# Optimization experiments

Measured on AMD Instinct MI355X. Metric: run time of the kernel, lower is better.

## Reference

```python
import jax, jax.numpy as jnp
import numpy as np

B, L, D_MODEL, N_HEADS = 2, 2048, 1024, 16
D_HEAD = D_MODEL // N_HEADS
EPS = 1e-5


def setup_inputs() -> dict:
    key = jax.random.key(0)
    ks = jax.random.split(key, 10)
    x = jax.random.normal(ks[0], (B, L, D_MODEL), dtype=jnp.float32)
    # causal boolean mask [B, L, L]
    attn_mask = jnp.broadcast_to(jnp.tril(jnp.ones((L, L), dtype=bool)), (B, L, L))
    ts = jax.random.randint(ks[1], (B, L), 0, 10000)
    rope_lambda = jax.random.uniform(ks[2], (B, L, 1), dtype=jnp.float32)
    q_gate = jax.random.uniform(ks[3], (B, L, N_HEADS), dtype=jnp.float32)
    k_gate = jax.random.uniform(ks[4], (B, L, N_HEADS), dtype=jnp.float32)
    v_gate = jax.random.uniform(ks[5], (B, L, N_HEADS), dtype=jnp.float32)
    type_pair_bias = jax.random.normal(ks[6], (B, 1, L, L), dtype=jnp.float32)
    # parameters (torch Linear convention: y = x @ W.T + b)
    proj_w = jax.random.normal(ks[7], (4 * D_MODEL, D_MODEL), dtype=jnp.float32) * 0.02
    proj_b = jnp.zeros((4 * D_MODEL,), dtype=jnp.float32)
    out_w = jax.random.normal(ks[8], (D_MODEL, D_MODEL), dtype=jnp.float32) * 0.02
    out_b = jnp.zeros((D_MODEL,), dtype=jnp.float32)
    head_scale = jnp.ones((N_HEADS,), dtype=jnp.float32) * (D_HEAD ** -0.5)
    ln_gamma = jnp.ones((D_MODEL,), dtype=jnp.float32)
    ln_beta = jnp.zeros((D_MODEL,), dtype=jnp.float32)
    return {"x": x, "attn_mask": attn_mask, "ts": ts, "rope_lambda": rope_lambda,
            "q_gate": q_gate, "k_gate": k_gate, "v_gate": v_gate,
            "type_pair_bias": type_pair_bias, "proj_w": proj_w, "proj_b": proj_b,
            "out_w": out_w, "out_b": out_b, "head_scale": head_scale,
            "ln_gamma": ln_gamma, "ln_beta": ln_beta}


def _split_heads(t):
    b, l, _ = t.shape
    return t.reshape(b, l, N_HEADS, D_HEAD).transpose(0, 2, 1, 3)  # [B,H,L,Dh]


def _apply_rope(q, k, rope_lambda):
    # behavior-module RoPE: positions from cumsum of rope_lambda
    pos = jnp.cumsum(rope_lambda[..., 0], axis=1)  # [B, L]
    inv_freq = 1.0 / (10000.0 ** (jnp.arange(0, D_HEAD, 2, dtype=jnp.float32) / D_HEAD))
    freqs = pos[:, None, :, None] * inv_freq[None, None, None, :]  # [B,1,L,Dh/2]
    cos, sin = jnp.cos(freqs), jnp.sin(freqs)

    def rot(t):
        te, to = t[..., 0::2], t[..., 1::2]
        return jnp.concatenate([te * cos - to * sin, te * sin + to * cos], axis=-1)

    return rot(q), rot(k)


def reference(x, attn_mask, ts, rope_lambda, q_gate, k_gate, v_gate,
              type_pair_bias, proj_w, proj_b, out_w, out_b, head_scale,
              ln_gamma, ln_beta):
    b, l, d = x.shape
    h = jax.nn.silu(x @ proj_w.T + proj_b)  # [B,L,4D]
    u, v, q, k = jnp.split(h, 4, axis=-1)
    u, v, q, k = _split_heads(u), _split_heads(v), _split_heads(q), _split_heads(k)
    q, k = _apply_rope(q, k, rope_lambda)
    # multiplicative per-head gates: [B,L,H] -> [B,H,L,1]
    q = q * q_gate.transpose(0, 2, 1)[..., None]
    k = k * k_gate.transpose(0, 2, 1)[..., None]
    v = v * v_gate.transpose(0, 2, 1)[..., None]
    logits = jnp.einsum('bhid,bhjd->bhij', q, k)
    logits = logits * head_scale[None, :, None, None]
    # original does two adds: + type_pair_bias and + 3.0 * type_pair_bias
    logits = logits + type_pair_bias
    logits = logits + 3.0 * type_pair_bias
    logits = jax.nn.silu(logits)  # non-softmax SiLU attention
    logits = jnp.where(attn_mask[:, None, :, :], logits, 0.0)
    y = jnp.einsum('bhij,bhjd->bhid', logits, v)  # [B,H,L,Dh]
    y = y.transpose(0, 2, 1, 3).reshape(b, l, d)
    y = y * u.transpose(0, 2, 1, 3).reshape(b, l, d)  # gated output
    y = y @ out_w.T + out_b
    r = x + y  # dropout is identity in eval mode
    mu = jnp.mean(r, axis=-1, keepdims=True)
    var = jnp.mean((r - mu) ** 2, axis=-1, keepdims=True)
    return (r - mu) / jnp.sqrt(var + EPS) * ln_gamma + ln_beta
```

## Files before the change

kernel.cpp:

```cpp
#include <hip/hip_runtime.h>
#include <cstdint>
#include <cstddef>

typedef unsigned short u16;
typedef __attribute__((ext_vector_type(8))) short short8v;
typedef __attribute__((ext_vector_type(4))) float f32x4;

#define B_   2
#define L_   2048
#define D_   1024
#define NH_  16
#define DH_  64
#define M_   (B_*L_)
#define N4_  (4*D_)

__device__ __forceinline__ float bf2f(u16 u) {
  union { float f; unsigned int i; } v; v.i = ((unsigned int)u) << 16; return v.f;
}
__device__ __forceinline__ u16 f2bf(float f) {
  union { float f; unsigned int i; } v; v.f = f;
  unsigned int x = v.i;
  return (u16)((x + 0x7fffu + ((x >> 16) & 1u)) >> 16);
}
__device__ __forceinline__ unsigned int pk_bf16(float a, float b) {
#if __has_builtin(__builtin_amdgcn_cvt_pk_bf16_f32)
  auto r = __builtin_amdgcn_cvt_pk_bf16_f32(a, b);
  union { decltype(r) v; unsigned int u; } c; c.v = r; return c.u;
#else
  unsigned int r;
  asm("v_cvt_pk_bf16_f32 %0, %1, %2" : "=v"(r) : "v"(a), "v"(b));
  return r;
#endif
}
__device__ __forceinline__ float siluf(float x) {
  return x * __builtin_amdgcn_rcpf(1.0f + __expf(-x));
}

__device__ __forceinline__ void gl2lds16(const u16* g, u16* l) {
  __builtin_amdgcn_global_load_lds(
      (const __attribute__((address_space(1))) unsigned int*)(const void*)g,
      (__attribute__((address_space(3))) unsigned int*)(void*)l,
      16, 0, 0);
}

__global__ __launch_bounds__(256) void k_conv_cum(const float* __restrict__ x,
                                                  const float* __restrict__ pw,
                                                  const float* __restrict__ ow,
                                                  const float* __restrict__ lam,
                                                  u16* __restrict__ xb,
                                                  u16* __restrict__ pwb,
                                                  u16* __restrict__ owb,
                                                  float* __restrict__ pos) {
  const int NX = M_ * D_ / 4, NP = N4_ * D_ / 4;
  int bid = blockIdx.x;
  int tid = threadIdx.x;
  if (bid < 9216) {
    int i = bid * 256 + tid;
    const float* src; u16* dst; int j;
    if (i < NX)            { src = x;  dst = xb;  j = i; }
    else if (i < NX + NP)  { src = pw; dst = pwb; j = i - NX; }
    else                   { src = ow; dst = owb; j = i - NX - NP; }
    float4 v = ((const float4*)src)[j];
    ushort4 o; o.x = f2bf(v.x); o.y = f2bf(v.y); o.z = f2bf(v.z); o.w = f2bf(v.w);
    ((ushort4*)dst)[j] = o;
  } else {
    int b = bid - 9216;
    const float* in = lam + (size_t)b * L_;
    float* out = pos + (size_t)b * L_;
    float loc[8], s = 0.0f;
#pragma unroll
    for (int i = 0; i < 8; ++i) { loc[i] = in[tid * 8 + i]; s += loc[i]; }
    __shared__ float sb[256];
    sb[tid] = s;
    __syncthreads();
    for (int off = 1; off < 256; off <<= 1) {
      float t = (tid >= off) ? sb[tid - off] : 0.0f;
      __syncthreads();
      sb[tid] += t;
      __syncthreads();
    }
    float run = sb[tid] - s;
#pragma unroll
    for (int i = 0; i < 8; ++i) { run += loc[i]; out[tid * 8 + i] = run; }
  }
}

__global__ __launch_bounds__(256, 4) void k_gemm1(const u16* __restrict__ A,
                                                  const u16* __restrict__ Bw,
                                                  const float* __restrict__ bias,
                                                  u16* __restrict__ hu, u16* __restrict__ hv,
                                                  u16* __restrict__ hq, u16* __restrict__ hk) {
  const int K = D_;
  int bn = blockIdx.x, bm = blockIdx.y, tid = threadIdx.x;
  int w = tid >> 6, lane = tid & 63, quad = lane >> 4, r16 = lane & 15;
  __shared__ __align__(16) u16 As[8192], Bs[8192];
  const u16* gA = A  + (size_t)(bm * 128) * K;
  const u16* gB = Bw + (size_t)(bn * 128) * K;
  int srow = tid >> 2, sc = tid & 3;
#pragma unroll
  for (int s = 0; s < 2; ++s) {
    int row = s * 64 + srow;
    int q = (sc - (row >> 1)) & 3;
    gl2lds16(gA + (size_t)row * K + q * 8, As + s * 2048 + w * 512);
    gl2lds16(gB + (size_t)row * K + q * 8, Bs + s * 2048 + w * 512);
  }
  f32x4 acc[4][4] = {};
  int wm = w & 1, wn = w >> 1;
  const int rowb = wm * 64, colb = wn * 64;
  for (int n = 0; n < 32; ++n) {
    __syncthreads();
    if (n + 1 < 32) {
      int kt = (n + 1) * 32, pb = (n + 1) & 1;
#pragma unroll
      for (int s = 0; s < 2; ++s) {
        int row = s * 64 + srow;
        int q = (sc - (row >> 1)) & 3;
        gl2lds16(gA + (size_t)row * K + kt + q * 8, As + pb * 4096 + s * 2048 + w * 512);
        gl2lds16(gB + (size_t)row * K + kt + q * 8, Bs + pb * 4096 + s * 2048 + w * 512);
      }
    }
    const u16* Ab = As + (n & 1) * 4096;
    const u16* Bb = Bs + (n & 1) * 4096;
    short8v af[4], bf[4];
#pragma unroll
    for (int mi = 0; mi < 4; ++mi) {
      int row = rowb + mi * 16 + r16;
      af[mi] = *(const short8v*)(Ab + (row * 4 + ((quad + (row >> 1)) & 3)) * 8);
    }
#pragma unroll
    for (int ni = 0; ni < 4; ++ni) {
      int row = colb + ni * 16 + r16;
      bf[ni] = *(const short8v*)(Bb + (row * 4 + ((quad + (row >> 1)) & 3)) * 8);
    }
#pragma unroll
    for (int mi = 0; mi < 4; ++mi)
#pragma unroll
      for (int ni = 0; ni < 4; ++ni)
        acc[mi][ni] = __builtin_amdgcn_mfma_f32_16x16x32_bf16(af[mi], bf[ni], acc[mi][ni], 0, 0, 0);
  }
  int nb = (bn * 128) >> 10;
  u16* dst = (nb == 0) ? hu : (nb == 1) ? hv : (nb == 2) ? hq : hk;
  int cbase = (bn * 128) & 1023;
  int row0 = bm * 128 + rowb;
#pragma unroll
  for (int ni = 0; ni < 4; ++ni) {
    int gcol = bn * 128 + colb + ni * 16 + r16;
    int lcol = cbase + colb + ni * 16 + r16;
    float bb = bias[gcol];
#pragma unroll
    for (int mi = 0; mi < 4; ++mi)
#pragma unroll
      for (int r = 0; r < 4; ++r) {
        int row = row0 + mi * 16 + quad * 4 + r;
        dst[(size_t)row * D_ + lcol] = f2bf(siluf(acc[mi][ni][r] + bb));
      }
  }
}

__global__ __launch_bounds__(256) void k_rope_vt(const u16* __restrict__ hq, const u16* __restrict__ hk,
                                                 const u16* __restrict__ hv,
                                                 const float* __restrict__ pos,
                                                 const float* __restrict__ qg, const float* __restrict__ kg,
                                                 const float* __restrict__ vg,
                                                 const float* __restrict__ hsc,
                                                 u16* __restrict__ Qb, u16* __restrict__ Kb,
                                                 u16* __restrict__ Vtb) {
  int bid = blockIdx.x;
  int tid = threadIdx.x;
  if (bid < 2048) {
    int idx = bid * 256 + tid;
    int j4 = idx & 7;
    int l  = (idx >> 3) & 2047;
    int bh = idx >> 14;
    int b = bh >> 4, hh = bh & 15;
    int row = b * L_ + l;
    float p = pos[row];
    float qs = qg[(size_t)row * NH_ + hh] * hsc[hh];
    float kgv = kg[(size_t)row * NH_ + hh];
    const u16* hqr = hq + (size_t)row * D_ + hh * DH_ + j4 * 8;
    const u16* hkr = hk + (size_t)row * D_ + hh * DH_ + j4 * 8;
    short8v qv = *(const short8v*)hqr;
    short8v kv = *(const short8v*)hkr;
    size_t ob = ((size_t)bh * L_ + l) * DH_ + j4 * 4;
    u16 qeo[4], qoo[4], keo[4], koo[4];
#pragma unroll
    for (int t = 0; t < 4; ++t) {
      int j = j4 * 4 + t;
      float inv = __expf(-(float)j * 0.28782313662425574f);
      float a = p * inv;
      float c, s;
      __sincosf(a, &s, &c);
      float qe = bf2f((u16)qv[2 * t]), qo = bf2f((u16)qv[2 * t + 1]);
      float ke = bf2f((u16)kv[2 * t]), ko = bf2f((u16)kv[2 * t + 1]);
      qeo[t] = f2bf((qe * c - qo * s) * qs);
      qoo[t] = f2bf((qe * s + qo * c) * qs);
      keo[t] = f2bf((ke * c - ko * s) * kgv);
      koo[t] = f2bf((ke * s + ko * c) * kgv);
    }
    *(ushort4*)(Qb + ob)      = make_ushort4(qeo[0], qeo[1], qeo[2], qeo[3]);
    *(ushort4*)(Qb + ob + 32) = make_ushort4(qoo[0], qoo[1], qoo[2], qoo[3]);
    *(ushort4*)(Kb + ob)      = make_ushort4(keo[0], keo[1], keo[2], keo[3]);
    *(ushort4*)(Kb + ob + 32) = make_ushort4(koo[0], koo[1], koo[2], koo[3]);
  } else {
    int b2 = bid - 2048;
    int lt = b2 & 31;
    int bh = b2 >> 5;
    int b = bh >> 4, hh = bh & 15;
    __shared__ u16 t[64][68];
    {
      int r = tid >> 2, cg = tid & 3;
      int row = b * L_ + lt * 64 + r;
      float gv = vg[(size_t)row * NH_ + hh];
      const u16* src = hv + (size_t)row * D_ + hh * DH_ + cg * 16;
      short8v v0 = ((const short8v*)src)[0];
      short8v v1 = ((const short8v*)src)[1];
#pragma unroll
      for (int e = 0; e < 8; ++e) {
        t[r][cg * 16 + e]     = f2bf(bf2f((u16)v0[e]) * gv);
        t[r][cg * 16 + 8 + e] = f2bf(bf2f((u16)v1[e]) * gv);
      }
    }
    __syncthreads();
    {
      int d = tid >> 2, lg = tid & 3;
      short8v o0, o1;
#pragma unroll
      for (int e = 0; e < 8; ++e) o0[e] = (short)t[lg * 16 + e][d];
#pragma unroll
      for (int e = 0; e < 8; ++e) o1[e] = (short)t[lg * 16 + 8 + e][d];
      u16* dst = Vtb + ((size_t)bh * DH_ + d) * L_ + lt * 64 + lg * 16;
      ((short8v*)dst)[0] = o0;
      ((short8v*)dst)[1] = o1;
    }
  }
}

__global__ __launch_bounds__(256, 4) void k_attn(const u16* __restrict__ Qb, const u16* __restrict__ Kb,
                                                 const u16* __restrict__ Vtb, const float* __restrict__ tpb,
                                                 const u16* __restrict__ hu, u16* __restrict__ A2) {
  int id = blockIdx.x;
  int group = id >> 5, bh = id & 31;
  int i64 = (group & 1) ? (group >> 1) : (31 - (group >> 1));
  int jmax = i64 >> 1;
  int b = bh >> 4, hh = bh & 15;
  int tid = threadIdx.x, w = tid >> 6, lane = tid & 63, quad = lane >> 4, r16 = lane & 15;
  __shared__ __align__(16) u16 Ks[8192];
  __shared__ __align__(16) u16 Vs[8192];
  const size_t bhbase = (size_t)bh * L_ * DH_;
  int irow = i64 * 64 + w * 16;
  int gimax_w = irow + 15;
  const u16* qt = Qb + bhbase + (size_t)irow * DH_;
  short8v bq[2];
#pragma unroll
  for (int ks = 0; ks < 2; ++ks)
    bq[ks] = *(const short8v*)(qt + (size_t)r16 * DH_ + ks * 32 + quad * 8);
#pragma unroll
  for (int s = 0; s < 4; ++s) {
    int row = (s & 1) * 64 + (tid >> 2);
    int q = ((tid & 3) - (row >> 1)) & 3;
    gl2lds16(Kb + bhbase + (size_t)row * DH_ + (s >> 1) * 32 + q * 8, Ks + s * 2048 + w * 512);
  }
  const float* bpr = tpb + ((size_t)b * L_ + irow + r16) * L_ + quad * 4;
  float4 bv[8];
#pragma unroll
  for (int tj = 0; tj < 8; ++tj)
    if (tj * 16 <= gimax_w) bv[tj] = *(const float4*)(bpr + tj * 16);
  f32x4 accy[4] = {};
  for (int jt = 0; jt <= jmax; ++jt) {
    __syncthreads();
#pragma unroll
    for (int s = 0; s < 4; ++s) {
      int row = tid >> 2;
      int q = ((tid & 3) - (row >> 1)) & 3;
      gl2lds16(Vtb + bhbase + (size_t)row * L_ + jt * 128 + s * 32 + q * 8, Vs + s * 2048 + w * 512);
    }
    unsigned int paw[4][4];
#pragma unroll
    for (int ks2 = 0; ks2 < 4; ++ks2) {
      if (jt * 128 + ks2 * 32 > gimax_w) continue;
      unsigned int W[2][2];
#pragma unroll
      for (int t = 0; t < 2; ++t) {
        int tj = 2 * ks2 + t;
        int jlo = jt * 128 + tj * 16;
        unsigned int p01 = 0, p23 = 0;
        if (jlo <= gimax_w) {
          int row = tj * 16 + r16;
          int sw = (quad + (row >> 1)) & 3;
          short8v ak0 = *(const short8v*)(Ks + (row * 4 + sw) * 8);
          short8v ak1 = *(const short8v*)(Ks + 4096 + (row * 4 + sw) * 8);
          f32x4 acc = {};
          acc = __builtin_amdgcn_mfma_f32_16x16x32_bf16(ak0, bq[0], acc, 0, 0, 0);
          acc = __builtin_amdgcn_mfma_f32_16x16x32_bf16(ak1, bq[1], acc, 0, 0, 0);
          int gi = irow + r16;
          int j0 = jlo + quad * 4;
          float4 bvv = bv[tj];
          float v0 = (j0     <= gi) ? siluf(fmaf(4.0f, bvv.x, acc[0])) : 0.0f;
          float v1 = (j0 + 1 <= gi) ? siluf(fmaf(4.0f, bvv.y, acc[1])) : 0.0f;
          float v2 = (j0 + 2 <= gi) ? siluf(fmaf(4.0f, bvv.z, acc[2])) : 0.0f;
          float v3 = (j0 + 3 <= gi) ? siluf(fmaf(4.0f, bvv.w, acc[3])) : 0.0f;
          p01 = pk_bf16(v0, v1);
          p23 = pk_bf16(v2, v3);
        }
        W[t][0] = p01; W[t][1] = p23;
      }
#pragma unroll
      for (int p = 0; p < 2; ++p) {
        unsigned int x = W[0][p], y = W[1][p];
        asm("v_permlane32_swap_b32 %0, %1" : "+v"(x), "+v"(y));
        asm("v_permlane16_swap_b32 %0, %1" : "+v"(x), "+v"(y));
        paw[ks2][p]     = x;
        paw[ks2][2 + p] = y;
      }
    }
    __syncthreads();
    if (jt < jmax) {
      const size_t kb = bhbase + (size_t)(jt + 1) * 128 * DH_;
#pragma unroll
      for (int s = 0; s < 4; ++s) {
        int row = (s & 1) * 64 + (tid >> 2);
        int q = ((tid & 3) - (row >> 1)) & 3;
        gl2lds16(Kb + kb + (size_t)row * DH_ + (s >> 1) * 32 + q * 8, Ks + s * 2048 + w * 512);
      }
      int jn = (jt + 1) * 128;
#pragma unroll
      for (int tj = 0; tj < 8; ++tj)
        if (jn + tj * 16 <= gimax_w) bv[tj] = *(const float4*)(bpr + jn + tj * 16);
    }
#pragma unroll
    for (int ks = 0; ks < 4; ++ks) {
      if (jt * 128 + ks * 32 > gimax_w) continue;
      union { unsigned int u[4]; short8v s; } pu;
      pu.u[0] = paw[ks][0]; pu.u[1] = paw[ks][1]; pu.u[2] = paw[ks][2]; pu.u[3] = paw[ks][3];
      short8v pa = pu.s;
#pragma unroll
      for (int ni = 0; ni < 4; ++ni) {
        int row = ni * 16 + r16;
        short8v vb = *(const short8v*)(Vs + ks * 2048 + (row * 4 + ((quad + (row >> 1)) & 3)) * 8);
        accy[ni] = __builtin_amdgcn_mfma_f32_16x16x32_bf16(pa, vb, accy[ni], 0, 0, 0);
      }
    }
  }
#pragma unroll
  for (int ni = 0; ni < 4; ++ni) {
    int d = ni * 16 + r16;
#pragma unroll
    for (int r = 0; r < 4; ++r) {
      int lr = w * 16 + quad * 4 + r;
      size_t rowg = (size_t)b * L_ + (size_t)i64 * 64 + lr;
      float u = bf2f(hu[rowg * D_ + hh * DH_ + d]);
      A2[rowg * D_ + hh * DH_ + d] = f2bf(accy[ni][r] * u);
    }
  }
}

__global__ __launch_bounds__(256, 4) void k_gemm2(const u16* __restrict__ A,
                                                  const u16* __restrict__ Bw,
                                                  const float* __restrict__ bias,
                                                  const float* __restrict__ xres,
                                                  float* __restrict__ out) {
  const int K = D_;
  int bn = blockIdx.x, bm = blockIdx.y, tid = threadIdx.x;
  int w = tid >> 6, lane = tid & 63, quad = lane >> 4, r16 = lane & 15;
  __shared__ __align__(16) u16 As[8192], Bs[8192];
  const u16* gA = A  + (size_t)(bm * 128) * K;
  const u16* gB = Bw + (size_t)(bn * 128) * K;
  int srow = tid >> 2, sc = tid & 3;
#pragma unroll
  for (int s = 0; s < 2; ++s) {
    int row = s * 64 + srow;
    int q = (sc - (row >> 1)) & 3;
    gl2lds16(gA + (size_t)row * K + q * 8, As + s * 2048 + w * 512);
    gl2lds16(gB + (size_t)row * K + q * 8, Bs + s * 2048 + w * 512);
  }
  f32x4 acc[4][4] = {};
  int wm = w & 1, wn = w >> 1;
  const int rowb = wm * 64, colb = wn * 64;
  for (int n = 0; n < 32; ++n) {
    __syncthreads();
    if (n + 1 < 32) {
      int kt = (n + 1) * 32, pb = (n + 1) & 1;
#pragma unroll
      for (int s = 0; s < 2; ++s) {
        int row = s * 64 + srow;
        int q = (sc - (row >> 1)) & 3;
        gl2lds16(gA + (size_t)row * K + kt + q * 8, As + pb * 4096 + s * 2048 + w * 512);
        gl2lds16(gB + (size_t)row * K + kt + q * 8, Bs + pb * 4096 + s * 2048 + w * 512);
      }
    }
    const u16* Ab = As + (n & 1) * 4096;
    const u16* Bb = Bs + (n & 1) * 4096;
    short8v af[4], bf[4];
#pragma unroll
    for (int mi = 0; mi < 4; ++mi) {
      int row = rowb + mi * 16 + r16;
      af[mi] = *(const short8v*)(Ab + (row * 4 + ((quad + (row >> 1)) & 3)) * 8);
    }
#pragma unroll
    for (int ni = 0; ni < 4; ++ni) {
      int row = colb + ni * 16 + r16;
      bf[ni] = *(const short8v*)(Bb + (row * 4 + ((quad + (row >> 1)) & 3)) * 8);
    }
#pragma unroll
    for (int mi = 0; mi < 4; ++mi)
#pragma unroll
      for (int ni = 0; ni < 4; ++ni)
        acc[mi][ni] = __builtin_amdgcn_mfma_f32_16x16x32_bf16(af[mi], bf[ni], acc[mi][ni], 0, 0, 0);
  }
  int row0 = bm * 128 + rowb, col0 = bn * 128 + colb;
#pragma unroll
  for (int ni = 0; ni < 4; ++ni) {
    int col = col0 + ni * 16 + r16;
    float bb = bias[col];
#pragma unroll
    for (int mi = 0; mi < 4; ++mi)
#pragma unroll
      for (int r = 0; r < 4; ++r) {
        int row = row0 + mi * 16 + quad * 4 + r;
        out[(size_t)row * D_ + col] = acc[mi][ni][r] + bb + xres[(size_t)row * D_ + col];
      }
  }
}

__global__ __launch_bounds__(256) void k_ln(float* __restrict__ r,
                                            const float* __restrict__ g,
                                            const float* __restrict__ be) {
  int row = blockIdx.x, tid = threadIdx.x;
  float* pr = r + (size_t)row * D_;
  __shared__ float s1[4], s2[4];
  float v[4];
#pragma unroll
  for (int i = 0; i < 4; ++i) v[i] = pr[i * 256 + tid];
  float s = v[0] + v[1] + v[2] + v[3];
#pragma unroll
  for (int o = 32; o > 0; o >>= 1) s += __shfl_down(s, o, 64);
  if ((tid & 63) == 0) s1[tid >> 6] = s;
  __syncthreads();
  float mu = (s1[0] + s1[1] + s1[2] + s1[3]) * (1.0f / D_);
  float d = 0.0f;
#pragma unroll
  for (int i = 0; i < 4; ++i) { float t = v[i] - mu; d += t * t; }
#pragma unroll
  for (int o = 32; o > 0; o >>= 1) d += __shfl_down(d, o, 64);
  if ((tid & 63) == 0) s2[tid >> 6] = d;
  __syncthreads();
  float var = (s2[0] + s2[1] + s2[2] + s2[3]) * (1.0f / D_);
  float inv = rsqrtf(var + 1e-5f);
#pragma unroll
  for (int i = 0; i < 4; ++i) {
    int c = i * 256 + tid;
    pr[c] = (v[i] - mu) * inv * g[c] + be[c];
  }
}

extern "C" void kernel_launch(void* const* d_in, const int* in_sizes, int n_in,
                              void* d_out, int out_size, void* d_ws, size_t ws_size,
                              hipStream_t stream) {
  const float* x   = (const float*)d_in[0];
  const float* lam = (const float*)d_in[3];
  const float* qg  = (const float*)d_in[4];
  const float* kg  = (const float*)d_in[5];
  const float* vg  = (const float*)d_in[6];
  const float* tpb = (const float*)d_in[7];
  const float* pw  = (const float*)d_in[8];
  const float* pb  = (const float*)d_in[9];
  const float* ow  = (const float*)d_in[10];
  const float* ob  = (const float*)d_in[11];
  const float* hsc = (const float*)d_in[12];
  const float* lng = (const float*)d_in[13];
  const float* lnb = (const float*)d_in[14];
  float* out = (float*)d_out;

  char* ws = (char*)d_ws;
  u16* xb   = (u16*)(ws + 0);
  u16* pwb  = (u16*)(ws + 8388608);
  u16* owb  = (u16*)(ws + 16777216);
  u16* hu   = (u16*)(ws + 18874368);
  u16* hv   = (u16*)(ws + 27262976);
  u16* hq   = (u16*)(ws + 35651584);
  u16* hk   = (u16*)(ws + 44040192);
  float* pos = (float*)(ws + 52428800);
  u16* Qb  = xb;
  u16* Kb  = pwb;
  u16* Vtb = hq;
  u16* A2  = hk;

  k_conv_cum<<<9218, 256, 0, stream>>>(x, pw, ow, lam, xb, pwb, owb, pos);
  k_gemm1<<<dim3(32, 32), 256, 0, stream>>>(xb, pwb, pb, hu, hv, hq, hk);
  k_rope_vt<<<3072, 256, 0, stream>>>(hq, hk, hv, pos, qg, kg, vg, hsc, Qb, Kb, Vtb);
  k_attn<<<1024, 256, 0, stream>>>(Qb, Kb, Vtb, tpb, hu, A2);
  k_gemm2<<<dim3(8, 32), 256, 0, stream>>>(A2, owb, ob, x, out);
  k_ln<<<4096, 256, 0, stream>>>(out, lng, lnb);
}
```

Measured before the change: 313.2 us.

## Restructure attention into single-wave blocks reading K/V directly from global memory

The attention kernel changes from 256-thread blocks that stage K and V tiles in shared memory under barriers to 64-thread single-wave blocks. Each wave handles 32 query rows, reads K/V fragments straight from global memory (relying on L2/cache), and maps blocks so that heads are spread across XCDs, with the longest causal rows scheduled first. It also adds a fast path for fully unmasked tiles that skips the per-element causal compare. This removes LDS staging and barrier stalls, but adds redundant global and L2 traffic, because every wave now loads K/V on its own.

```diff
diff --git a/kernel.cpp b/kernel.cpp
--- a/kernel.cpp
+++ b/kernel.cpp
@@ -235,123 +235,110 @@
   }
 }
 
-__global__ __launch_bounds__(256, 4) void k_attn(const u16* __restrict__ Qb, const u16* __restrict__ Kb,
-                                                 const u16* __restrict__ Vtb, const float* __restrict__ tpb,
-                                                 const u16* __restrict__ hu, u16* __restrict__ A2) {
+__global__ __launch_bounds__(64, 3) void k_attn(const u16* __restrict__ Qb, const u16* __restrict__ Kb,
+                                                const u16* __restrict__ Vtb, const float* __restrict__ tpb,
+                                                const u16* __restrict__ hu, u16* __restrict__ A2) {
   int id = blockIdx.x;
-  int group = id >> 5, bh = id & 31;
-  int i64 = (group & 1) ? (group >> 1) : (31 - (group >> 1));
-  int jmax = i64 >> 1;
+  int xcd = id & 7, rr_ = id >> 3;
+  int bh = xcd + 8 * (rr_ & 3);
+  int t  = 63 - (rr_ >> 2);
   int b = bh >> 4, hh = bh & 15;
-  int tid = threadIdx.x, w = tid >> 6, lane = tid & 63, quad = lane >> 4, r16 = lane & 15;
-  __shared__ __align__(16) u16 Ks[8192];
-  __shared__ __align__(16) u16 Vs[8192];
+  int lane = threadIdx.x & 63, quad = lane >> 4, r16 = lane & 15;
   const size_t bhbase = (size_t)bh * L_ * DH_;
-  int irow = i64 * 64 + w * 16;
-  int gimax_w = irow + 15;
+  const int irow = t * 32;
+  const int gimax = irow + 31;
+  const int jmax = t >> 2;
   const u16* qt = Qb + bhbase + (size_t)irow * DH_;
-  short8v bq[2];
-#pragma unroll
-  for (int ks = 0; ks < 2; ++ks)
-    bq[ks] = *(const short8v*)(qt + (size_t)r16 * DH_ + ks * 32 + quad * 8);
-#pragma unroll
-  for (int s = 0; s < 4; ++s) {
-    int row = (s & 1) * 64 + (tid >> 2);
-    int q = ((tid & 3) - (row >> 1)) & 3;
-    gl2lds16(Kb + bhbase + (size_t)row * DH_ + (s >> 1) * 32 + q * 8, Ks + s * 2048 + w * 512);
-  }
-  const float* bpr = tpb + ((size_t)b * L_ + irow + r16) * L_ + quad * 4;
-  float4 bv[8];
-#pragma unroll
-  for (int tj = 0; tj < 8; ++tj)
-    if (tj * 16 <= gimax_w) bv[tj] = *(const float4*)(bpr + tj * 16);
-  f32x4 accy[4] = {};
+  short8v bq[2][2];
+#pragma unroll
+  for (int ti = 0; ti < 2; ++ti)
+#pragma unroll
+    for (int ks = 0; ks < 2; ++ks)
+      bq[ti][ks] = *(const short8v*)(qt + (size_t)(ti * 16 + r16) * DH_ + ks * 32 + quad * 8);
+  const u16* Kln = Kb + bhbase + (size_t)r16 * DH_ + quad * 8;
+  const u16* Vln = Vtb + bhbase + (size_t)r16 * L_ + quad * 8;
+  const float* bbase[2];
+#pragma unroll
+  for (int ti = 0; ti < 2; ++ti)
+    bbase[ti] = tpb + ((size_t)(b * L_ + irow + ti * 16 + r16)) * L_ + quad * 4;
+  f32x4 accy[2][4] = {};
   for (int jt = 0; jt <= jmax; ++jt) {
-    __syncthreads();
-#pragma unroll
-    for (int s = 0; s < 4; ++s) {
-      int row = tid >> 2;
-      int q = ((tid & 3) - (row >> 1)) & 3;
-      gl2lds16(Vtb + bhbase + (size_t)row * L_ + jt * 128 + s * 32 + q * 8, Vs + s * 2048 + w * 512);
-    }
-    unsigned int paw[4][4];
-#pragma unroll
-    for (int ks2 = 0; ks2 < 4; ++ks2) {
-      if (jt * 128 + ks2 * 32 > gimax_w) continue;
-      unsigned int W[2][2];
-#pragma unroll
-      for (int t = 0; t < 2; ++t) {
-        int tj = 2 * ks2 + t;
-        int jlo = jt * 128 + tj * 16;
-        unsigned int p01 = 0, p23 = 0;
-        if (jlo <= gimax_w) {
-          int row = tj * 16 + r16;
-          int sw = (quad + (row >> 1)) & 3;
-          short8v ak0 = *(const short8v*)(Ks + (row * 4 + sw) * 8);
-          short8v ak1 = *(const short8v*)(Ks + 4096 + (row * 4 + sw) * 8);
-          f32x4 acc = {};
-          acc = __builtin_amdgcn_mfma_f32_16x16x32_bf16(ak0, bq[0], acc, 0, 0, 0);
-          acc = __builtin_amdgcn_mfma_f32_16x16x32_bf16(ak1, bq[1], acc, 0, 0, 0);
-          int gi = irow + r16;
-          int j0 = jlo + quad * 4;
-          float4 bvv = bv[tj];
-          float v0 = (j0     <= gi) ? siluf(fmaf(4.0f, bvv.x, acc[0])) : 0.0f;
-          float v1 = (j0 + 1 <= gi) ? siluf(fmaf(4.0f, bvv.y, acc[1])) : 0.0f;
-          float v2 = (j0 + 2 <= gi) ? siluf(fmaf(4.0f, bvv.z, acc[2])) : 0.0f;
-          float v3 = (j0 + 3 <= gi) ? siluf(fmaf(4.0f, bvv.w, acc[3])) : 0.0f;
-          p01 = pk_bf16(v0, v1);
-          p23 = pk_bf16(v2, v3);
+    const u16* Kj = Kln + (size_t)(jt * 128) * DH_;
+    const u16* Vj = Vln + jt * 128;
+#pragma unroll
+    for (int ks = 0; ks < 4; ++ks) {
+      int jsl = jt * 128 + ks * 32;
+      if (jsl > gimax) continue;
+      unsigned int Wv[2][2][2];
+#pragma unroll
+      for (int st = 0; st < 2; ++st) {
+        int jlo = jsl + st * 16;
+        const u16* kp = Kj + (size_t)(ks * 2 + st) * 16 * DH_;
+        short8v ak0 = *(const short8v*)(kp);
+        short8v ak1 = *(const short8v*)(kp + 32);
+#pragma unroll
+        for (int ti = 0; ti < 2; ++ti) {
+          int gim = irow + ti * 16;
+          unsigned int p01 = 0, p23 = 0;
+          if (jlo <= gim + 15) {
+            f32x4 acc = {};
+            acc = __builtin_amdgcn_mfma_f32_16x16x32_bf16(ak0, bq[ti][0], acc, 0, 0, 0);
+            acc = __builtin_amdgcn_mfma_f32_16x16x32_bf16(ak1, bq[ti][1], acc, 0, 0, 0);
+            float4 bvv = *(const float4*)(bbase[ti] + jlo);
+            if (jlo + 15 <= gim) {
+              p01 = pk_bf16(siluf(fmaf(4.0f, bvv.x, acc[0])), siluf(fmaf(4.0f, bvv.y, acc[1])));
+              p23 = pk_bf16(siluf(fmaf(4.0f, bvv.z, acc[2])), siluf(fmaf(4.0f, bvv.w, acc[3])));
+            } else {
+              int gi = gim + r16;
+              int j0 = jlo + quad * 4;
+              float v0 = (j0     <= gi) ? siluf(fmaf(4.0f, bvv.x, acc[0])) : 0.0f;
+              float v1 = (j0 + 1 <= gi) ? siluf(fmaf(4.0f, bvv.y, acc[1])) : 0.0f;
+              float v2 = (j0 + 2 <= gi) ? siluf(fmaf(4.0f, bvv.z, acc[2])) : 0.0f;
+              float v3 = (j0 + 3 <= gi) ? siluf(fmaf(4.0f, bvv.w, acc[3])) : 0.0f;
+              p01 = pk_bf16(v0, v1);
+              p23 = pk_bf16(v2, v3);
+            }
+          }
+          Wv[st][ti][0] = p01; Wv[st][ti][1] = p23;
         }
-        W[t][0] = p01; W[t][1] = p23;
-      }
-#pragma unroll
-      for (int p = 0; p < 2; ++p) {
-        unsigned int x = W[0][p], y = W[1][p];
-        asm("v_permlane32_swap_b32 %0, %1" : "+v"(x), "+v"(y));
-        asm("v_permlane16_swap_b32 %0, %1" : "+v"(x), "+v"(y));
-        paw[ks2][p]     = x;
-        paw[ks2][2 + p] = y;
-      }
-    }
-    __syncthreads();
-    if (jt < jmax) {
-      const size_t kb = bhbase + (size_t)(jt + 1) * 128 * DH_;
-#pragma unroll
-      for (int s = 0; s < 4; ++s) {
-        int row = (s & 1) * 64 + (tid >> 2);
-        int q = ((tid & 3) - (row >> 1)) & 3;
-        gl2lds16(Kb + kb + (size_t)row * DH_ + (s >> 1) * 32 + q * 8, Ks + s * 2048 + w * 512);
-      }
-      int jn = (jt + 1) * 128;
-#pragma unroll
-      for (int tj = 0; tj < 8; ++tj)
-        if (jn + tj * 16 <= gimax_w) bv[tj] = *(const float4*)(bpr + jn + tj * 16);
-    }
-#pragma unroll
-    for (int ks = 0; ks < 4; ++ks) {
-      if (jt * 128 + ks * 32 > gimax_w) continue;
-      union { unsigned int u[4]; short8v s; } pu;
-      pu.u[0] = paw[ks][0]; pu.u[1] = paw[ks][1]; pu.u[2] = paw[ks][2]; pu.u[3] = paw[ks][3];
-      short8v pa = pu.s;
+      }
+      unsigned int paw[2][4];
+#pragma unroll
+      for (int ti = 0; ti < 2; ++ti)
+#pragma unroll
+        for (int p = 0; p < 2; ++p) {
+          unsigned int x = Wv[0][ti][p], y = Wv[1][ti][p];
+          asm("v_permlane32_swap_b32 %0, %1" : "+v"(x), "+v"(y));
+          asm("v_permlane16_swap_b32 %0, %1" : "+v"(x), "+v"(y));
+          paw[ti][p]     = x;
+          paw[ti][2 + p] = y;
+        }
 #pragma unroll
       for (int ni = 0; ni < 4; ++ni) {
-        int row = ni * 16 + r16;
-        short8v vb = *(const short8v*)(Vs + ks * 2048 + (row * 4 + ((quad + (row >> 1)) & 3)) * 8);
-        accy[ni] = __builtin_amdgcn_mfma_f32_16x16x32_bf16(pa, vb, accy[ni], 0, 0, 0);
-      }
-    }
-  }
-#pragma unroll
-  for (int ni = 0; ni < 4; ++ni) {
-    int d = ni * 16 + r16;
-#pragma unroll
-    for (int r = 0; r < 4; ++r) {
-      int lr = w * 16 + quad * 4 + r;
-      size_t rowg = (size_t)b * L_ + (size_t)i64 * 64 + lr;
-      float u = bf2f(hu[rowg * D_ + hh * DH_ + d]);
-      A2[rowg * D_ + hh * DH_ + d] = f2bf(accy[ni][r] * u);
-    }
-  }
+        short8v vb = *(const short8v*)(Vj + (size_t)ni * 16 * L_ + ks * 32);
+#pragma unroll
+        for (int ti = 0; ti < 2; ++ti) {
+          union { unsigned int u[4]; short8v s; } pu;
+          pu.u[0] = paw[ti][0]; pu.u[1] = paw[ti][1]; pu.u[2] = paw[ti][2]; pu.u[3] = paw[ti][3];
+          accy[ti][ni] = __builtin_amdgcn_mfma_f32_16x16x32_bf16(pu.s, vb, accy[ti][ni], 0, 0, 0);
+        }
+      }
+    }
+  }
+  const u16* hup = hu + ((size_t)(b * L_ + irow)) * D_ + hh * DH_;
+  u16* a2p = A2 + ((size_t)(b * L_ + irow)) * D_ + hh * DH_;
+#pragma unroll
+  for (int ti = 0; ti < 2; ++ti)
+#pragma unroll
+    for (int ni = 0; ni < 4; ++ni) {
+      int d = ni * 16 + r16;
+#pragma unroll
+      for (int rreg = 0; rreg < 4; ++rreg) {
+        int lr = ti * 16 + quad * 4 + rreg;
+        float u = bf2f(hup[(size_t)lr * D_ + d]);
+        a2p[(size_t)lr * D_ + d] = f2bf(accy[ti][ni][rreg] * u);
+      }
+    }
 }
 
 __global__ __launch_bounds__(256, 4) void k_gemm2(const u16* __restrict__ A,
@@ -488,7 +475,7 @@
   k_conv_cum<<<9218, 256, 0, stream>>>(x, pw, ow, lam, xb, pwb, owb, pos);
   k_gemm1<<<dim3(32, 32), 256, 0, stream>>>(xb, pwb, pb, hu, hv, hq, hk);
   k_rope_vt<<<3072, 256, 0, stream>>>(hq, hk, hv, pos, qg, kg, vg, hsc, Qb, Kb, Vtb);
-  k_attn<<<1024, 256, 0, stream>>>(Qb, Kb, Vtb, tpb, hu, A2);
+  k_attn<<<2048, 64, 0, stream>>>(Qb, Kb, Vtb, tpb, hu, A2);
   k_gemm2<<<dim3(8, 32), 256, 0, stream>>>(A2, owb, ob, x, out);
   k_ln<<<4096, 256, 0, stream>>>(out, lng, lnb);
 }
```

After: 377.1 us. +20.4%, slower.
